# Kernel optimization log

Hardware: AMD Instinct MI355X
Metric: run time of the kernel (lower is better)

The kernel has to match this reference:

```python
import jax, jax.numpy as jnp
import numpy as np

N, F_IN, F_OUT, HEADS = 8192, 128, 64, 2
NEG_INF = -1e10
LEAKY_ALPHA = 0.2


def setup_inputs() -> dict:
    key = jax.random.key(0)
    k_x, k_a, k_w, k_as, k_an = jax.random.split(key, 5)
    X = jax.random.normal(k_x, (N, F_IN), dtype=jnp.float32)
    A = (jax.random.uniform(k_a, (N, N)) < 0.004).astype(jnp.float32)
    A = jnp.maximum(A, jnp.eye(N, dtype=jnp.float32))
    kernels = jax.random.normal(k_w, (HEADS, F_IN, F_OUT), dtype=jnp.float32) * (1.0 / np.sqrt(F_IN))
    biases = jnp.zeros((HEADS, F_OUT), dtype=jnp.float32)
    attn_self = jax.random.normal(k_as, (HEADS, F_OUT), dtype=jnp.float32) * (1.0 / np.sqrt(F_OUT))
    attn_neigh = jax.random.normal(k_an, (HEADS, F_OUT), dtype=jnp.float32) * (1.0 / np.sqrt(F_OUT))
    return {"X": X, "A": A, "kernels": kernels, "biases": biases,
            "attn_self": attn_self, "attn_neigh": attn_neigh}


def reference(X, A, kernels, biases, attn_self, attn_neigh):
    # per-head linear projection: [H, N, F_OUT]
    feats = jnp.einsum('nf,hfo->hno', X, kernels)
    # additive attention logits (GAT): e_ij = leakyrelu(a_s^T h_i + a_n^T h_j)
    a_s = jnp.einsum('hno,ho->hn', feats, attn_self)    # [H, N]
    a_n = jnp.einsum('hno,ho->hn', feats, attn_neigh)   # [H, N]
    dense = a_s[:, :, None] + a_n[:, None, :]           # [H, N, N]
    dense = jnp.where(dense > 0, dense, LEAKY_ALPHA * dense)
    dense = dense + NEG_INF * (1.0 - A)                 # adjacency mask
    attn = jax.nn.softmax(dense, axis=-1)               # [H, N, N]
    # dropout_rate = 0.0 -> dropout is identity
    node_feats = jnp.einsum('hnm,hmo->hno', attn, feats) + biases[:, None, :]
    out = jnp.mean(node_feats, axis=0)                  # 'average' head reduction
    return jax.nn.relu(out)                             # activation='relu'
```

## Files before the change

kernel.cpp:

```cpp
#include <hip/hip_runtime.h>
#include <hip/hip_bf16.h>
#include <cfloat>

#define N_NODES 8192
#define F_IN    128
#define F_OUT   64
#define HEADS   2
#define LEAKY   0.2f
#define ROWS    8
#define CAP     128

typedef float f32x4 __attribute__((ext_vector_type(4)));

__global__ __launch_bounds__(128) void feats_kernel(
    const float* __restrict__ X, const float* __restrict__ W,
    const float* __restrict__ attn_self, const float* __restrict__ attn_neigh,
    float* __restrict__ feats, float* __restrict__ a_s, float* __restrict__ a_n)
{
    __shared__ float Xs[ROWS][F_IN];
    const int tid = threadIdx.x;
    const int n0  = blockIdx.x * ROWS;

    for (int k = tid; k < ROWS * F_IN; k += 128) {
        Xs[k / F_IN][k % F_IN] = X[(size_t)(n0 + k / F_IN) * F_IN + (k % F_IN)];
    }
    __syncthreads();

    const int h = tid >> 6;
    const int o = tid & 63;
    const float* Wh = W + (size_t)h * F_IN * F_OUT;

    float acc[ROWS];
    #pragma unroll
    for (int r = 0; r < ROWS; ++r) acc[r] = 0.f;

    for (int f = 0; f < F_IN; ++f) {
        float wv = Wh[f * F_OUT + o];
        #pragma unroll
        for (int r = 0; r < ROWS; ++r) acc[r] += Xs[r][f] * wv;
    }

    const float asv = attn_self[h * F_OUT + o];
    const float anv = attn_neigh[h * F_OUT + o];
    #pragma unroll
    for (int r = 0; r < ROWS; ++r) {
        const int n = n0 + r;
        const float v = acc[r];
        feats[((size_t)n * 2 + h) * F_OUT + o] = v;
        float s = v * asv;
        float t = v * anv;
        #pragma unroll
        for (int off = 32; off > 0; off >>= 1) {
            s += __shfl_down(s, off);
            t += __shfl_down(t, off);
        }
        if (o == 0) {
            a_s[n * 2 + h] = s;
            a_n[n * 2 + h] = t;
        }
    }
}

__global__ __launch_bounds__(256) void fused_row_kernel(
    const float* __restrict__ A, const float* __restrict__ feats,
    const float* __restrict__ a_s, const float* __restrict__ a_n,
    const float* __restrict__ biases, float* __restrict__ out)
{
    __shared__ int   jj_s[4][CAP];
    __shared__ float w0_s[4][CAP];
    __shared__ float w1_s[4][CAP];

    const int wave = threadIdx.x >> 6;
    const int lane = threadIdx.x & 63;
    const int row  = blockIdx.x * 4 + wave;

    int*   jj = jj_s[wave];
    float* w0 = w0_s[wave];
    float* w1 = w1_s[wave];

    const unsigned long long lt = (1ULL << lane) - 1ULL;

    const f32x4* Arow = (const f32x4*)(A + (size_t)row * N_NODES);
    f32x4 buf[2][4];
    #pragma unroll
    for (int q = 0; q < 4; ++q)
        buf[0][q] = __builtin_nontemporal_load(&Arow[q * 64 + lane]);

    int base = 0;
    #pragma unroll
    for (int g = 0; g < 8; ++g) {
        const int cb = g & 1, nb = cb ^ 1;
        if (g < 7) {
            #pragma unroll
            for (int q = 0; q < 4; ++q)
                buf[nb][q] = __builtin_nontemporal_load(
                    &Arow[(g + 1) * 256 + q * 64 + lane]);
        }
        #pragma unroll
        for (int q = 0; q < 4; ++q) {
            const f32x4 v = buf[cb][q];
            const int col0 = (g * 256 + q * 64 + lane) * 4;
            #pragma unroll
            for (int comp = 0; comp < 4; ++comp) {
                const bool nz = v[comp] > 0.5f;
                const unsigned long long m = __ballot(nz);
                if (nz) {
                    const int p = base + __popcll(m & lt);
                    if (p < CAP) jj[p] = col0 + comp;
                }
                base += __popcll(m);
            }
        }
    }
    const int count = min(base, CAP);

    const float2 as = ((const float2*)a_s)[row];
    float m0 = -FLT_MAX, m1 = -FLT_MAX;
    for (int k = lane; k < count; k += 64) {
        const float2 an = ((const float2*)a_n)[jj[k]];
        float e0 = as.x + an.x;  e0 = e0 > 0.f ? e0 : LEAKY * e0;
        float e1 = as.y + an.y;  e1 = e1 > 0.f ? e1 : LEAKY * e1;
        w0[k] = e0; w1[k] = e1;
        m0 = fmaxf(m0, e0); m1 = fmaxf(m1, e1);
    }
    #pragma unroll
    for (int off = 32; off > 0; off >>= 1) {
        m0 = fmaxf(m0, __shfl_xor(m0, off));
        m1 = fmaxf(m1, __shfl_xor(m1, off));
    }
    float s0 = 0.f, s1 = 0.f;
    for (int k = lane; k < count; k += 64) {
        const float p0 = __expf(w0[k] - m0); w0[k] = p0; s0 += p0;
        const float p1 = __expf(w1[k] - m1); w1[k] = p1; s1 += p1;
    }
    #pragma unroll
    for (int off = 32; off > 0; off >>= 1) {
        s0 += __shfl_xor(s0, off);
        s1 += __shfl_xor(s1, off);
    }

    float acc0 = 0.f, acc1 = 0.f;
    int k = 0;
    for (; k + 1 < count; k += 2) {
        const int j0 = jj[k], j1 = jj[k + 1];
        const float* r0 = feats + (size_t)j0 * 128;
        const float* r1 = feats + (size_t)j1 * 128;
        const float p00 = w0[k],     p10 = w1[k];
        const float p01 = w0[k + 1], p11 = w1[k + 1];
        const float f00 = r0[lane], f01 = r0[64 + lane];
        const float f10 = r1[lane], f11 = r1[64 + lane];
        acc0 += p00 * f00; acc1 += p10 * f01;
        acc0 += p01 * f10; acc1 += p11 * f11;
    }
    if (k < count) {
        const int j = jj[k];
        const float* r = feats + (size_t)j * 128;
        acc0 += w0[k] * r[lane];
        acc1 += w1[k] * r[64 + lane];
    }
    const float v = 0.5f * ((acc0 / s0 + biases[lane]) +
                            (acc1 / s1 + biases[F_OUT + lane]));
    out[(size_t)row * F_OUT + lane] = v > 0.f ? v : 0.f;
}

extern "C" void kernel_launch(void* const* d_in, const int* in_sizes, int n_in,
                              void* d_out, int out_size, void* d_ws, size_t ws_size,
                              hipStream_t stream) {
    const float* X          = (const float*)d_in[0];
    const float* A          = (const float*)d_in[1];
    const float* W          = (const float*)d_in[2];
    const float* biases     = (const float*)d_in[3];
    const float* attn_self  = (const float*)d_in[4];
    const float* attn_neigh = (const float*)d_in[5];
    float* out = (float*)d_out;

    float* feats = (float*)d_ws;
    float* a_s   = feats + (size_t)HEADS * N_NODES * F_OUT;
    float* a_n   = a_s + HEADS * N_NODES;

    feats_kernel<<<N_NODES / ROWS, 128, 0, stream>>>(
        X, W, attn_self, attn_neigh, feats, a_s, a_n);
    fused_row_kernel<<<N_NODES / 4, 256, 0, stream>>>(
        A, feats, a_s, a_n, biases, out);
}
```

Measured before the change: 370.2 us.

## Overlap adjacency bitmap compression with feature projection in a merged first kernel

Adjacency scanning moves out of the row kernel into a first kernel that interleaves blocks: four of every five compress four rows of A into 64-bit ballot bitmaps, the fifth computes projected features for sixteen nodes. The row kernel then rebuilds neighbor lists from the bitmap with a prefix scan and bit iteration. Features are stored head-interleaved so each lane fetches a float2 per neighbor. The goal is to overlap the bandwidth-bound A read with the feature GEMM and shorten the latency-bound row kernel, at the cost of writing and rereading a bitmap plus extra scan work.

```diff
diff --git a/kernel.cpp b/kernel.cpp
--- a/kernel.cpp
+++ b/kernel.cpp
@@ -1,5 +1,4 @@
 #include <hip/hip_runtime.h>
-#include <hip/hip_bf16.h>
 #include <cfloat>
 
 #define N_NODES 8192
@@ -7,46 +6,91 @@
 #define F_OUT   64
 #define HEADS   2
 #define LEAKY   0.2f
-#define ROWS    8
 #define CAP     128
+#define FROWS   16
+#define MPR     (N_NODES / 64)
 
 typedef float f32x4 __attribute__((ext_vector_type(4)));
 
-__global__ __launch_bounds__(128) void feats_kernel(
+__device__ __forceinline__ void compress_rows(
+    const float* __restrict__ A, unsigned long long* __restrict__ bmp, int cb)
+{
+    const int wave = threadIdx.x >> 6;
+    const int lane = threadIdx.x & 63;
+    const int row  = cb * 4 + wave;
+
+    const f32x4* Arow = (const f32x4*)(A + (size_t)row * N_NODES);
+    unsigned long long* brow = bmp + (size_t)row * MPR;
+
+    f32x4 buf[2][4];
+    #pragma unroll
+    for (int q = 0; q < 4; ++q)
+        buf[0][q] = __builtin_nontemporal_load(&Arow[q * 64 + lane]);
+
+    #pragma unroll
+    for (int g = 0; g < 8; ++g) {
+        const int cur = g & 1, nxt = cur ^ 1;
+        if (g < 7) {
+            #pragma unroll
+            for (int q = 0; q < 4; ++q)
+                buf[nxt][q] = __builtin_nontemporal_load(
+                    &Arow[(g + 1) * 256 + q * 64 + lane]);
+        }
+        #pragma unroll
+        for (int q = 0; q < 4; ++q) {
+            const f32x4 v = buf[cur][q];
+            const unsigned long long m0 = __ballot(v[0] > 0.5f);
+            const unsigned long long m1 = __ballot(v[1] > 0.5f);
+            const unsigned long long m2 = __ballot(v[2] > 0.5f);
+            const unsigned long long m3 = __ballot(v[3] > 0.5f);
+            ulonglong2 st;
+            st.x = (lane == 0) ? m0 : m2;
+            st.y = (lane == 0) ? m1 : m3;
+            if (lane < 2)
+                ((ulonglong2*)(brow + (size_t)(g * 4 + q) * 4))[lane] = st;
+        }
+    }
+}
+
+__device__ __forceinline__ void feats_rows(
     const float* __restrict__ X, const float* __restrict__ W,
     const float* __restrict__ attn_self, const float* __restrict__ attn_neigh,
-    float* __restrict__ feats, float* __restrict__ a_s, float* __restrict__ a_n)
-{
-    __shared__ float Xs[ROWS][F_IN];
-    const int tid = threadIdx.x;
-    const int n0  = blockIdx.x * ROWS;
-
-    for (int k = tid; k < ROWS * F_IN; k += 128) {
-        Xs[k / F_IN][k % F_IN] = X[(size_t)(n0 + k / F_IN) * F_IN + (k % F_IN)];
+    float* __restrict__ feats, float* __restrict__ a_s, float* __restrict__ a_n,
+    float* Xs, int fb)
+{
+    const int n0 = fb * FROWS;
+    {
+        f32x4* dst = (f32x4*)Xs;
+        const f32x4* src = (const f32x4*)(X + (size_t)n0 * F_IN);
+        for (int k = threadIdx.x; k < FROWS * F_IN / 4; k += 256)
+            dst[k] = src[k];
     }
     __syncthreads();
 
-    const int h = tid >> 6;
-    const int o = tid & 63;
+    const int wave = threadIdx.x >> 6;
+    const int lane = threadIdx.x & 63;
+    const int h    = wave & 1;
+    const int r0   = (wave >> 1) * 8;
     const float* Wh = W + (size_t)h * F_IN * F_OUT;
 
-    float acc[ROWS];
-    #pragma unroll
-    for (int r = 0; r < ROWS; ++r) acc[r] = 0.f;
+    float acc[8];
+    #pragma unroll
+    for (int r = 0; r < 8; ++r) acc[r] = 0.f;
 
     for (int f = 0; f < F_IN; ++f) {
-        float wv = Wh[f * F_OUT + o];
+        const float wv = Wh[f * F_OUT + lane];
         #pragma unroll
-        for (int r = 0; r < ROWS; ++r) acc[r] += Xs[r][f] * wv;
-    }
-
-    const float asv = attn_self[h * F_OUT + o];
-    const float anv = attn_neigh[h * F_OUT + o];
-    #pragma unroll
-    for (int r = 0; r < ROWS; ++r) {
-        const int n = n0 + r;
+        for (int r = 0; r < 8; ++r)
+            acc[r] += Xs[(r0 + r) * F_IN + f] * wv;
+    }
+
+    const float asv = attn_self[h * F_OUT + lane];
+    const float anv = attn_neigh[h * F_OUT + lane];
+    #pragma unroll
+    for (int r = 0; r < 8; ++r) {
+        const int n = n0 + r0 + r;
         const float v = acc[r];
-        feats[((size_t)n * 2 + h) * F_OUT + o] = v;
+        feats[((size_t)n * F_OUT + lane) * 2 + h] = v;
         float s = v * asv;
         float t = v * anv;
         #pragma unroll
@@ -54,15 +98,31 @@
             s += __shfl_down(s, off);
             t += __shfl_down(t, off);
         }
-        if (o == 0) {
+        if (lane == 0) {
             a_s[n * 2 + h] = s;
             a_n[n * 2 + h] = t;
         }
     }
 }
 
+__global__ __launch_bounds__(256) void stage1_kernel(
+    const float* __restrict__ X, const float* __restrict__ A,
+    const float* __restrict__ W,
+    const float* __restrict__ attn_self, const float* __restrict__ attn_neigh,
+    float* __restrict__ feats, float* __restrict__ a_s, float* __restrict__ a_n,
+    unsigned long long* __restrict__ bmp)
+{
+    __shared__ float Xs[FROWS * F_IN];
+    const int bid = blockIdx.x;
+    if ((bid % 5) == 4) {
+        feats_rows(X, W, attn_self, attn_neigh, feats, a_s, a_n, Xs, bid / 5);
+    } else {
+        compress_rows(A, bmp, (bid / 5) * 4 + (bid % 5));
+    }
+}
+
 __global__ __launch_bounds__(256) void fused_row_kernel(
-    const float* __restrict__ A, const float* __restrict__ feats,
+    const unsigned long long* __restrict__ bmp, const float* __restrict__ feats,
     const float* __restrict__ a_s, const float* __restrict__ a_n,
     const float* __restrict__ biases, float* __restrict__ out)
 {
@@ -78,41 +138,31 @@
     float* w0 = w0_s[wave];
     float* w1 = w1_s[wave];
 
-    const unsigned long long lt = (1ULL << lane) - 1ULL;
-
-    const f32x4* Arow = (const f32x4*)(A + (size_t)row * N_NODES);
-    f32x4 buf[2][4];
-    #pragma unroll
-    for (int q = 0; q < 4; ++q)
-        buf[0][q] = __builtin_nontemporal_load(&Arow[q * 64 + lane]);
-
-    int base = 0;
-    #pragma unroll
-    for (int g = 0; g < 8; ++g) {
-        const int cb = g & 1, nb = cb ^ 1;
-        if (g < 7) {
-            #pragma unroll
-            for (int q = 0; q < 4; ++q)
-                buf[nb][q] = __builtin_nontemporal_load(
-                    &Arow[(g + 1) * 256 + q * 64 + lane]);
-        }
-        #pragma unroll
-        for (int q = 0; q < 4; ++q) {
-            const f32x4 v = buf[cb][q];
-            const int col0 = (g * 256 + q * 64 + lane) * 4;
-            #pragma unroll
-            for (int comp = 0; comp < 4; ++comp) {
-                const bool nz = v[comp] > 0.5f;
-                const unsigned long long m = __ballot(nz);
-                if (nz) {
-                    const int p = base + __popcll(m & lt);
-                    if (p < CAP) jj[p] = col0 + comp;
-                }
-                base += __popcll(m);
-            }
-        }
-    }
-    const int count = min(base, CAP);
+    const ulonglong2 mm =
+        ((const ulonglong2*)(bmp + (size_t)row * MPR))[lane];
+    const int cnt = __popcll(mm.x) + __popcll(mm.y);
+    int x = cnt;
+    #pragma unroll
+    for (int off = 1; off < 64; off <<= 1) {
+        const int y = __shfl_up(x, off);
+        if (lane >= off) x += y;
+    }
+    const int total = __shfl(x, 63);
+    int p = x - cnt;
+    const int jbase = (lane >> 1) * 256 + (lane & 1) * 2;
+    unsigned long long m = mm.x;
+    while (m) {
+        const int b = __builtin_ctzll(m); m &= m - 1;
+        if (p < CAP) jj[p] = jbase + 4 * b;
+        ++p;
+    }
+    m = mm.y;
+    while (m) {
+        const int b = __builtin_ctzll(m); m &= m - 1;
+        if (p < CAP) jj[p] = jbase + 4 * b + 1;
+        ++p;
+    }
+    const int count = min(total, CAP);
 
     const float2 as = ((const float2*)a_s)[row];
     float m0 = -FLT_MAX, m1 = -FLT_MAX;
@@ -139,24 +189,20 @@
         s1 += __shfl_xor(s1, off);
     }
 
+    const float2* f2 = (const float2*)feats;
     float acc0 = 0.f, acc1 = 0.f;
     int k = 0;
     for (; k + 1 < count; k += 2) {
         const int j0 = jj[k], j1 = jj[k + 1];
-        const float* r0 = feats + (size_t)j0 * 128;
-        const float* r1 = feats + (size_t)j1 * 128;
-        const float p00 = w0[k],     p10 = w1[k];
-        const float p01 = w0[k + 1], p11 = w1[k + 1];
-        const float f00 = r0[lane], f01 = r0[64 + lane];
-        const float f10 = r1[lane], f11 = r1[64 + lane];
-        acc0 += p00 * f00; acc1 += p10 * f01;
-        acc0 += p01 * f10; acc1 += p11 * f11;
+        const float2 fa = f2[(size_t)j0 * F_OUT + lane];
+        const float2 fb = f2[(size_t)j1 * F_OUT + lane];
+        acc0 += w0[k] * fa.x;     acc1 += w1[k] * fa.y;
+        acc0 += w0[k + 1] * fb.x; acc1 += w1[k + 1] * fb.y;
     }
     if (k < count) {
-        const int j = jj[k];
-        const float* r = feats + (size_t)j * 128;
-        acc0 += w0[k] * r[lane];
-        acc1 += w1[k] * r[64 + lane];
+        const float2 fa = f2[(size_t)jj[k] * F_OUT + lane];
+        acc0 += w0[k] * fa.x;
+        acc1 += w1[k] * fa.y;
     }
     const float v = 0.5f * ((acc0 / s0 + biases[lane]) +
                             (acc1 / s1 + biases[F_OUT + lane]));
@@ -177,9 +223,11 @@
     float* feats = (float*)d_ws;
     float* a_s   = feats + (size_t)HEADS * N_NODES * F_OUT;
     float* a_n   = a_s + HEADS * N_NODES;
-
-    feats_kernel<<<N_NODES / ROWS, 128, 0, stream>>>(
-        X, W, attn_self, attn_neigh, feats, a_s, a_n);
+    unsigned long long* bmp =
+        (unsigned long long*)(a_n + HEADS * N_NODES);
+
+    stage1_kernel<<<2560, 256, 0, stream>>>(
+        X, A, W, attn_self, attn_neigh, feats, a_s, a_n, bmp);
     fused_row_kernel<<<N_NODES / 4, 256, 0, stream>>>(
-        A, feats, a_s, a_n, biases, out);
-}
+        bmp, feats, a_s, a_n, biases, out);
+}
```

New measurement: 366.2 us. No clear change (-1.1%).
